# Kernel tuning notes

Hardware: AMD Instinct MI355X
Metric: run time of the kernel (lower is better)

Reference implementation:

```python
import jax, jax.numpy as jnp
import numpy as np

B, C, F = 4, 3, 5
HO, WO = 256, 256
HI, WI = HO + F - 1, WO + F - 1


def setup_inputs() -> dict:
    key = jax.random.key(0)
    k = jax.random.split(key, 6)
    return {
        "tensorInput": jax.random.normal(k[0], (B, C, HI, WI), dtype=jnp.float32),
        "tensorVertical": jax.random.uniform(k[1], (B, F, HO, WO), dtype=jnp.float32),
        "tensorHorizontal": jax.random.uniform(k[2], (B, F, HO, WO), dtype=jnp.float32),
        "tensorOffsetX": jax.random.normal(k[3], (B, F * F, HO, WO), dtype=jnp.float32),
        "tensorOffsetY": jax.random.normal(k[4], (B, F * F, HO, WO), dtype=jnp.float32),
        "tensorMask": jax.random.uniform(k[5], (B, F * F, HO, WO), dtype=jnp.float32),
    }


def _dsepconv(inp, vertical, horizontal, offset_x, offset_y, mask):
    b, c, hin, win = inp.shape
    f = vertical.shape[1]
    ho, wo = vertical.shape[2], vertical.shape[3]
    half = (f - 1) / 2.0

    fy = jnp.arange(f, dtype=inp.dtype).reshape(f, 1, 1, 1)
    fx = jnp.arange(f, dtype=inp.dtype).reshape(1, f, 1, 1)
    hg = jnp.arange(ho, dtype=inp.dtype).reshape(1, 1, ho, 1)
    wg = jnp.arange(wo, dtype=inp.dtype).reshape(1, 1, 1, wo)

    off_y = offset_y.reshape(b, f, f, ho, wo)  # note: code uses offset_y for delta_x
    off_x = offset_x.reshape(b, f, f, ho, wo)  # and offset_x for delta_y

    # sample positions per tap, [B,F,F,Ho,Wo]
    px = jnp.clip(off_y + wg + fx - half + 1.0, 0.0, win - 1)
    py = jnp.clip(off_x + hg + fy - half + 1.0, 0.0, hin - 1)

    left_f = jnp.floor(px)
    top_f = jnp.floor(py)
    wx = 1.0 - (px - left_f)  # bilinear weights
    wy = 1.0 - (py - top_f)

    l = left_f.astype(jnp.int32)
    t = top_f.astype(jnp.int32)
    r = jnp.minimum(l + 1, win - 1)
    btm = jnp.minimum(t + 1, hin - 1)

    def gather(img, yi, xi):
        return img[:, yi, xi]

    g = jax.vmap(gather)
    v_tl = g(inp, t, l)
    v_tr = g(inp, t, r)
    v_bl = g(inp, btm, l)
    v_br = g(inp, btm, r)

    wx_ = wx[:, None]  # add channel axis -> [B,1,F,F,Ho,Wo]
    wy_ = wy[:, None]
    val = (v_tl * wx_ * wy_ + v_tr * (1 - wx_) * wy_
           + v_bl * wx_ * (1 - wy_) + v_br * (1 - wx_) * (1 - wy_))

    # separable filter x mask per tap: [B,F,F,Ho,Wo]
    w_tap = vertical[:, :, None] * horizontal[:, None, :] * mask.reshape(b, f, f, ho, wo)
    # accumulate over the F*F taps
    return jnp.sum(val * w_tap[:, None], axis=(2, 3))  # [B,C,Ho,Wo]


def reference(tensorInput, tensorVertical, tensorHorizontal, tensorOffsetX, tensorOffsetY, tensorMask):
    return _dsepconv(tensorInput, tensorVertical, tensorHorizontal,
                     tensorOffsetX, tensorOffsetY, tensorMask)
```

## Files before the change

### kernel.cpp

```cpp
#include <hip/hip_runtime.h>
#include <hip/hip_fp16.h>

constexpr int B  = 4;
constexpr int C  = 3;
constexpr int F  = 5;
constexpr int HO = 256;
constexpr int WO = 256;
constexpr int HI = HO + F - 1;
constexpr int WI = WO + F - 1;
constexpr int P  = HO * WO;
constexpr int FF = F * F;
constexpr int PI = HI * WI;

constexpr int TROWS = 19;
constexpr int TCOLS = 145;
constexpr int TSTRIDE = 149;
constexpr int TN = TROWS * TCOLS;
constexpr int AMAX = (TROWS - 2) * TSTRIDE + (TCOLS - 2);

__device__ __forceinline__ float2 ld2(const float* p) {
    return *reinterpret_cast<const float2*>(p);
}

__device__ __forceinline__ uint2 pack3(float a, float b, float c) {
    __half2 ab = __floats2half2_rn(a, b);
    __half2 cz = __floats2half2_rn(c, 0.0f);
    uint2 r;
    r.x = *reinterpret_cast<const unsigned int*>(&ab);
    r.y = *reinterpret_cast<const unsigned int*>(&cz);
    return r;
}

__device__ __forceinline__ void fmacc(uint2 v, float w,
                                      float& a0, float& a1, float& a2) {
    __half2 ab = *reinterpret_cast<const __half2*>(&v.x);
    __half2 cz = *reinterpret_cast<const __half2*>(&v.y);
    a0 += __half2float(__low2half(ab))  * w;
    a1 += __half2float(__high2half(ab)) * w;
    a2 += __half2float(__low2half(cz))  * w;
}

__global__ __launch_bounds__(256, 4) void dsepconv_kernel(
    const float* __restrict__ inp,
    const float* __restrict__ vert,
    const float* __restrict__ horz,
    const float* __restrict__ offX,
    const float* __restrict__ offY,
    const float* __restrict__ mask,
    float* __restrict__ out)
{
    __shared__ uint2 tileq[TROWS * TSTRIDE];
    __shared__ float red[2][3][128];

    const int tid  = threadIdx.x;
    const int lane = tid & 63;
    const int wave = tid >> 6;
    const int wrow = wave >> 1;
    const int half = wave & 1;

    const int bx   = blockIdx.x;
    const int x0   = (bx & 1) * 128;
    const int y0   = ((bx >> 1) & 127) * 2;
    const int b    = bx >> 8;

    const float* in0 = inp + (size_t)b * C * PI;
    const float* in1 = in0 + PI;
    const float* in2 = in1 + PI;

    const int x   = x0 + 2 * lane;
    const int y   = y0 + wrow;
    const int pix = y * WO + x;

    const float* offXb = offX + (size_t)b * FF * P + pix;
    const float* offYb = offY + (size_t)b * FF * P + pix;
    const float* maskb = mask + (size_t)b * FF * P + pix;
    const float* vb    = vert + (size_t)b * F * P + pix;
    const float* hb    = horz + (size_t)b * F * P + pix;

    const int k0 = half ? 12 : 0;
    const int k1 = half ? 25 : 12;

    float2 oy, ox, m, h, v;
    {
        const int i = k0 / F, j = k0 - (k0 / F) * F;
        oy = ld2(offYb + (size_t)k0 * P);
        ox = ld2(offXb + (size_t)k0 * P);
        m  = ld2(maskb + (size_t)k0 * P);
        h  = ld2(hb + (size_t)j * P);
        v  = ld2(vb + (size_t)i * P);
    }

    const int ry0 = y0 - 7;
    const int cx0 = x0 - 7;
#pragma unroll 1
    for (int e = tid; e < TN; e += 256) {
        int trow = e / TCOLS;
        int tcol = e - trow * TCOLS;
        int gy = min(max(ry0 + trow, 0), HI - 1);
        int gx = min(max(cx0 + tcol, 0), WI - 1);
        int g = gy * WI + gx;
        tileq[trow * TSTRIDE + tcol] = pack3(in0[g], in1[g], in2[g]);
    }
    __syncthreads();

    float acc0a = 0.f, acc1a = 0.f, acc2a = 0.f;
    float acc0b = 0.f, acc1b = 0.f, acc2b = 0.f;

#pragma unroll 1
    for (int k = k0; k < k1; ++k) {
        const int i = k / F;
        const int j = k - i * F;

        const int kn  = (k + 1 < k1) ? k + 1 : k;
        const int in_ = kn / F;
        const int jn  = kn - in_ * F;
        float2 oy_n = ld2(offYb + (size_t)kn * P);
        float2 ox_n = ld2(offXb + (size_t)kn * P);
        float2 m_n  = ld2(maskb + (size_t)kn * P);
        float2 h_n  = ld2(hb + (size_t)jn * P);
        float2 v_n  = ld2(vb + (size_t)in_ * P);

        float pya = fminf(fmaxf(ox.x + (float)(y + i - 1), 0.0f), (float)(HI - 1));
        float pyb = fminf(fmaxf(ox.y + (float)(y + i - 1), 0.0f), (float)(HI - 1));
        float pxa = fminf(fmaxf(oy.x + (float)(x + j - 1), 0.0f), (float)(WI - 1));
        float pxb = fminf(fmaxf(oy.y + (float)(x + j), 0.0f), (float)(WI - 1));

        float lfa = floorf(pxa), tfa = floorf(pya);
        float lfb = floorf(pxb), tfb = floorf(pyb);
        int la = (int)lfa, ta = (int)tfa;
        int lb = (int)lfb, tb = (int)tfb;
        float wxa = 1.0f - (pxa - lfa), wya = 1.0f - (pya - tfa);
        float wxb = 1.0f - (pxb - lfb), wyb = 1.0f - (pyb - tfb);

        int lta = ta - ry0, lla = la - cx0;
        int ltb = tb - ry0, llb = lb - cx0;
        bool oka = ((unsigned)lta <= TROWS - 2) & ((unsigned)lla <= TCOLS - 2);
        bool okb = ((unsigned)ltb <= TROWS - 2) & ((unsigned)llb <= TCOLS - 2);

        int aa = min(max(lta * TSTRIDE + lla, 0), AMAX);
        int ab = min(max(ltb * TSTRIDE + llb, 0), AMAX);

        uint2 ga0 = tileq[aa];
        uint2 ga1 = tileq[aa + 1];
        uint2 ga2 = tileq[aa + TSTRIDE];
        uint2 ga3 = tileq[aa + TSTRIDE + 1];
        uint2 gb0 = tileq[ab];
        uint2 gb1 = tileq[ab + 1];
        uint2 gb2 = tileq[ab + TSTRIDE];
        uint2 gb3 = tileq[ab + TSTRIDE + 1];

        if (__any(!(oka & okb))) {
            if (!oka) {
                int r  = min(la + 1, WI - 1);
                int bt = min(ta + 1, HI - 1);
                int o0 = ta * WI + la, o1 = ta * WI + r;
                int o2 = bt * WI + la, o3 = bt * WI + r;
                ga0 = pack3(in0[o0], in1[o0], in2[o0]);
                ga1 = pack3(in0[o1], in1[o1], in2[o1]);
                ga2 = pack3(in0[o2], in1[o2], in2[o2]);
                ga3 = pack3(in0[o3], in1[o3], in2[o3]);
            }
            if (!okb) {
                int r  = min(lb + 1, WI - 1);
                int bt = min(tb + 1, HI - 1);
                int o0 = tb * WI + lb, o1 = tb * WI + r;
                int o2 = bt * WI + lb, o3 = bt * WI + r;
                gb0 = pack3(in0[o0], in1[o0], in2[o0]);
                gb1 = pack3(in0[o1], in1[o1], in2[o1]);
                gb2 = pack3(in0[o2], in1[o2], in2[o2]);
                gb3 = pack3(in0[o3], in1[o3], in2[o3]);
            }
        }

        float wA   = v.x * h.x * m.x;
        float wywA = wya * wA;
        float wbwA = wA - wywA;
        float wtlA = wxa * wywA;
        float wtrA = wywA - wtlA;
        float wblA = wxa * wbwA;
        float wbrA = wbwA - wblA;

        float wB   = v.y * h.y * m.y;
        float wywB = wyb * wB;
        float wbwB = wB - wywB;
        float wtlB = wxb * wywB;
        float wtrB = wywB - wtlB;
        float wblB = wxb * wbwB;
        float wbrB = wbwB - wblB;

        fmacc(ga0, wtlA, acc0a, acc1a, acc2a);
        fmacc(ga1, wtrA, acc0a, acc1a, acc2a);
        fmacc(ga2, wblA, acc0a, acc1a, acc2a);
        fmacc(ga3, wbrA, acc0a, acc1a, acc2a);
        fmacc(gb0, wtlB, acc0b, acc1b, acc2b);
        fmacc(gb1, wtrB, acc0b, acc1b, acc2b);
        fmacc(gb2, wblB, acc0b, acc1b, acc2b);
        fmacc(gb3, wbrB, acc0b, acc1b, acc2b);

        oy = oy_n; ox = ox_n; m = m_n; h = h_n; v = v_n;
    }

    if (half) {
        *reinterpret_cast<float2*>(&red[wrow][0][2 * lane]) = make_float2(acc0a, acc0b);
        *reinterpret_cast<float2*>(&red[wrow][1][2 * lane]) = make_float2(acc1a, acc1b);
        *reinterpret_cast<float2*>(&red[wrow][2][2 * lane]) = make_float2(acc2a, acc2b);
    }
    __syncthreads();

    if (!half) {
        float* ob = out + (size_t)b * C * P + pix;
        float2 r0 = *reinterpret_cast<const float2*>(&red[wrow][0][2 * lane]);
        float2 r1 = *reinterpret_cast<const float2*>(&red[wrow][1][2 * lane]);
        float2 r2 = *reinterpret_cast<const float2*>(&red[wrow][2][2 * lane]);
        *reinterpret_cast<float2*>(&ob[0])     = make_float2(acc0a + r0.x, acc0b + r0.y);
        *reinterpret_cast<float2*>(&ob[P])     = make_float2(acc1a + r1.x, acc1b + r1.y);
        *reinterpret_cast<float2*>(&ob[2 * P]) = make_float2(acc2a + r2.x, acc2b + r2.y);
    }
}

extern "C" void kernel_launch(void* const* d_in, const int* in_sizes, int n_in,
                              void* d_out, int out_size, void* d_ws, size_t ws_size,
                              hipStream_t stream) {
    const float* inp  = (const float*)d_in[0];
    const float* vert = (const float*)d_in[1];
    const float* horz = (const float*)d_in[2];
    const float* offX = (const float*)d_in[3];
    const float* offY = (const float*)d_in[4];
    const float* mask = (const float*)d_in[5];
    float* out = (float*)d_out;

    dim3 block(256);
    dim3 grid(B * (HO / 2) * (WO / 128));
    dsepconv_kernel<<<grid, block, 0, stream>>>(inp, vert, horz, offX, offY, mask, out);
}
```

Before: 24.75 us.

## Prefetch per-tap streams two iterations ahead and shrink shared input tile halo

Replaces the one-ahead register prefetch of offsets, mask and filter values with a two-deep software pipeline, so global load latency has more loop work to hide behind. It also shrinks the shared-memory input tile halo from 7 to 6 pixels (19x145 to 17x143), reducing tile fill loads. Pixels sampled outside the smaller tile fall back to the slower direct global gather path more often. The deeper prefetch adds roughly ten live registers under the 256x4 launch bound.

```diff
diff --git a/kernel.cpp b/kernel.cpp
--- a/kernel.cpp
+++ b/kernel.cpp
@@ -12,8 +12,8 @@
 constexpr int FF = F * F;
 constexpr int PI = HI * WI;
 
-constexpr int TROWS = 19;
-constexpr int TCOLS = 145;
+constexpr int TROWS = 17;
+constexpr int TCOLS = 143;
 constexpr int TSTRIDE = 149;
 constexpr int TN = TROWS * TCOLS;
 constexpr int AMAX = (TROWS - 2) * TSTRIDE + (TCOLS - 2);
@@ -38,6 +38,25 @@
     a0 += __half2float(__low2half(ab))  * w;
     a1 += __half2float(__high2half(ab)) * w;
     a2 += __half2float(__low2half(cz))  * w;
+}
+
+struct Streams {
+    float2 oy, ox, mk, h, v;
+};
+
+__device__ __forceinline__ void loadStreams(
+    int k, Streams& s,
+    const float* __restrict__ offYb, const float* __restrict__ offXb,
+    const float* __restrict__ maskb, const float* __restrict__ vb,
+    const float* __restrict__ hb)
+{
+    const int i = k / F;
+    const int j = k - i * F;
+    s.oy = ld2(offYb + (size_t)k * P);
+    s.ox = ld2(offXb + (size_t)k * P);
+    s.mk = ld2(maskb + (size_t)k * P);
+    s.h  = ld2(hb + (size_t)j * P);
+    s.v  = ld2(vb + (size_t)i * P);
 }
 
 __global__ __launch_bounds__(256, 4) void dsepconv_kernel(
@@ -77,21 +96,16 @@
     const float* vb    = vert + (size_t)b * F * P + pix;
     const float* hb    = horz + (size_t)b * F * P + pix;
 
-    const int k0 = half ? 12 : 0;
-    const int k1 = half ? 25 : 12;
-
-    float2 oy, ox, m, h, v;
-    {
-        const int i = k0 / F, j = k0 - (k0 / F) * F;
-        oy = ld2(offYb + (size_t)k0 * P);
-        ox = ld2(offXb + (size_t)k0 * P);
-        m  = ld2(maskb + (size_t)k0 * P);
-        h  = ld2(hb + (size_t)j * P);
-        v  = ld2(vb + (size_t)i * P);
-    }
-
-    const int ry0 = y0 - 7;
-    const int cx0 = x0 - 7;
+    const int k0    = half ? 12 : 0;
+    const int k1    = half ? 25 : 12;
+    const int klast = k1 - 1;
+
+    Streams cur, n1, n2;
+    loadStreams(k0, cur, offYb, offXb, maskb, vb, hb);
+    loadStreams(min(k0 + 1, klast), n1, offYb, offXb, maskb, vb, hb);
+
+    const int ry0 = y0 - 6;
+    const int cx0 = x0 - 6;
 #pragma unroll 1
     for (int e = tid; e < TN; e += 256) {
         int trow = e / TCOLS;
@@ -111,19 +125,12 @@
         const int i = k / F;
         const int j = k - i * F;
 
-        const int kn  = (k + 1 < k1) ? k + 1 : k;
-        const int in_ = kn / F;
-        const int jn  = kn - in_ * F;
-        float2 oy_n = ld2(offYb + (size_t)kn * P);
-        float2 ox_n = ld2(offXb + (size_t)kn * P);
-        float2 m_n  = ld2(maskb + (size_t)kn * P);
-        float2 h_n  = ld2(hb + (size_t)jn * P);
-        float2 v_n  = ld2(vb + (size_t)in_ * P);
-
-        float pya = fminf(fmaxf(ox.x + (float)(y + i - 1), 0.0f), (float)(HI - 1));
-        float pyb = fminf(fmaxf(ox.y + (float)(y + i - 1), 0.0f), (float)(HI - 1));
-        float pxa = fminf(fmaxf(oy.x + (float)(x + j - 1), 0.0f), (float)(WI - 1));
-        float pxb = fminf(fmaxf(oy.y + (float)(x + j), 0.0f), (float)(WI - 1));
+        loadStreams(min(k + 2, klast), n2, offYb, offXb, maskb, vb, hb);
+
+        float pya = fminf(fmaxf(cur.ox.x + (float)(y + i - 1), 0.0f), (float)(HI - 1));
+        float pyb = fminf(fmaxf(cur.ox.y + (float)(y + i - 1), 0.0f), (float)(HI - 1));
+        float pxa = fminf(fmaxf(cur.oy.x + (float)(x + j - 1), 0.0f), (float)(WI - 1));
+        float pxb = fminf(fmaxf(cur.oy.y + (float)(x + j), 0.0f), (float)(WI - 1));
 
         float lfa = floorf(pxa), tfa = floorf(pya);
         float lfb = floorf(pxb), tfb = floorf(pyb);
@@ -172,7 +179,7 @@
             }
         }
 
-        float wA   = v.x * h.x * m.x;
+        float wA   = cur.v.x * cur.h.x * cur.mk.x;
         float wywA = wya * wA;
         float wbwA = wA - wywA;
         float wtlA = wxa * wywA;
@@ -180,7 +187,7 @@
         float wblA = wxa * wbwA;
         float wbrA = wbwA - wblA;
 
-        float wB   = v.y * h.y * m.y;
+        float wB   = cur.v.y * cur.h.y * cur.mk.y;
         float wywB = wyb * wB;
         float wbwB = wB - wywB;
         float wtlB = wxb * wywB;
@@ -197,7 +204,8 @@
         fmacc(gb2, wblB, acc0b, acc1b, acc2b);
         fmacc(gb3, wbrB, acc0b, acc1b, acc2b);
 
-        oy = oy_n; ox = ox_n; m = m_n; h = h_n; v = v_n;
+        cur = n1;
+        n1  = n2;
     }
 
     if (half) {
```

After: 25.38 us. +2.5%, slower.
